# Optimization experiments

Hardware: AMD Instinct MI355X
Metric: run time of the kernel (lower is better)

## Reference

```python
import jax, jax.numpy as jnp
import numpy as np

EMB = 1024
HEADS = 16
HEAD_DIM = EMB // HEADS
FF = 4 * EMB
B, S = 4, 2048


def gelu_tanh(x):
    c = jnp.sqrt(jnp.asarray(2.0 / jnp.pi, x.dtype))
    return 0.5 * x * (1.0 + jnp.tanh(c * (x + 0.044715 * x ** 3)))


def layernorm(x, g, b, eps=1e-5):
    mu = jnp.mean(x, axis=-1, keepdims=True)
    var = jnp.var(x, axis=-1, keepdims=True)
    return (x - mu) * jax.lax.rsqrt(var + eps) * g + b


def setup_inputs() -> dict:
    key = jax.random.key(0)
    ks = jax.random.split(key, 12)
    s = 0.02
    return {
        "x": jax.random.normal(ks[0], (B, S, EMB), jnp.float32),
        "Wq": jax.random.normal(ks[1], (EMB, EMB), jnp.float32) * s,
        "bq": jnp.zeros((EMB,), jnp.float32),
        "Wk": jax.random.normal(ks[2], (EMB, EMB), jnp.float32) * s,
        "bk": jnp.zeros((EMB,), jnp.float32),
        "Wv": jax.random.normal(ks[3], (EMB, EMB), jnp.float32) * s,
        "bv": jnp.zeros((EMB,), jnp.float32),
        "Wo": jax.random.normal(ks[4], (EMB, EMB), jnp.float32) * s,
        "bo": jnp.zeros((EMB,), jnp.float32),
        "W1": jax.random.normal(ks[5], (EMB, FF), jnp.float32) * s,
        "b1": jnp.zeros((FF,), jnp.float32),
        "W2": jax.random.normal(ks[6], (FF, EMB), jnp.float32) * s,
        "b2": jnp.zeros((EMB,), jnp.float32),
        "g1": jnp.ones((EMB,), jnp.float32),
        "be1": jnp.zeros((EMB,), jnp.float32),
        "g2": jnp.ones((EMB,), jnp.float32),
        "be2": jnp.zeros((EMB,), jnp.float32),
    }


def reference(x, Wq, bq, Wk, bk, Wv, bv, Wo, bo, W1, b1, W2, b2, g1, be1, g2, be2):
    b, s, _ = x.shape
    shortcut = x
    h = layernorm(x, g1, be1)
    # QKV projections -> [b, heads, s, head_dim]
    def proj(W, bias):
        return (h @ W + bias).reshape(b, s, HEADS, HEAD_DIM).transpose(0, 2, 1, 3)
    q, k, v = proj(Wq, bq), proj(Wk, bk), proj(Wv, bv)
    scores = jnp.einsum('bhqd,bhkd->bhqk', q, k) / jnp.sqrt(jnp.asarray(HEAD_DIM, x.dtype))
    causal = jnp.triu(jnp.ones((s, s), bool), k=1)  # True above diagonal -> masked
    scores = jnp.where(causal, -jnp.inf, scores)
    probs = jax.nn.softmax(scores, axis=-1)  # dropout p=0 -> identity
    ctx = jnp.einsum('bhqk,bhkd->bhqd', probs, v).transpose(0, 2, 1, 3).reshape(b, s, EMB)
    attn_out = ctx @ Wo + bo
    x = attn_out + shortcut
    shortcut = x
    h = layernorm(x, g2, be2)
    ff = gelu_tanh(h @ W1 + b1) @ W2 + b2
    return ff + shortcut
```

## Files before the change

kernel.cpp:

```cpp
#include <hip/hip_runtime.h>
#include <hip/hip_bf16.h>

#define EMB 1024
#define HEADS 16
#define HDIM 64
#define FFDIM 4096
#define BSZ 4
#define SEQ 2048
#define MROWS (BSZ * SEQ)
#define QKVW 3072
#define VSTRIDE 2080

typedef __attribute__((ext_vector_type(8))) short bf16x8;
typedef __attribute__((ext_vector_type(4))) float f32x4;
typedef __attribute__((ext_vector_type(16))) float f32x16;
typedef __attribute__((ext_vector_type(4))) unsigned short u16x4;
typedef unsigned short u16;

__device__ __forceinline__ float bf2f(u16 u) {
  union { unsigned int i; float f; } c; c.i = ((unsigned int)u) << 16; return c.f;
}
__device__ __forceinline__ u16 f2bf(float f) {
  union { float f; unsigned int i; } c; c.f = f;
  unsigned int i = c.i + 0x7fff + ((c.i >> 16) & 1);
  return (u16)(i >> 16);
}
__device__ __forceinline__ unsigned fbits(float f) {
  union { float f; unsigned u; } c; c.f = f; return c.u;
}
__device__ __forceinline__ unsigned pk2(float e0, float e1) {
  return (fbits(e0) >> 16) | (fbits(e1) & 0xffff0000u);
}
__device__ __forceinline__ f32x16 zero16() {
  f32x16 z;
#pragma unroll
  for (int i = 0; i < 16; ++i) z[i] = 0.f;
  return z;
}
__device__ __forceinline__ void gload16(const u16* g, void* lds) {
  __builtin_amdgcn_global_load_lds(
      (const __attribute__((address_space(1))) void*)g,
      (__attribute__((address_space(3))) void*)lds, 16, 0, 0);
}

__global__ __launch_bounds__(256) void ln_kernel(
    const float* __restrict__ x, const float* __restrict__ g,
    const float* __restrict__ be, u16* __restrict__ out) {
  int w = threadIdx.x >> 6, l = threadIdx.x & 63;
  size_t row = (size_t)blockIdx.x * 4 + w;
  const float* xr = x + row * EMB;
  float f[4][4];
  float s = 0.f, s2 = 0.f;
#pragma unroll
  for (int c = 0; c < 4; ++c) {
    f32x4 v = *(const f32x4*)(xr + c * 256 + l * 4);
#pragma unroll
    for (int j = 0; j < 4; ++j) {
      f[c][j] = v[j];
      s += v[j];
      s2 += v[j] * v[j];
    }
  }
#pragma unroll
  for (int m = 1; m < 64; m <<= 1) {
    s  += __shfl_xor(s, m);
    s2 += __shfl_xor(s2, m);
  }
  float mu = s * (1.f / EMB);
  float var = s2 * (1.f / EMB) - mu * mu;
  float rs = rsqrtf(var + 1e-5f);
#pragma unroll
  for (int c = 0; c < 4; ++c) {
    u16x4 o;
#pragma unroll
    for (int j = 0; j < 4; ++j) {
      int col = c * 256 + l * 4 + j;
      o[j] = f2bf((f[c][j] - mu) * rs * g[col] + be[col]);
    }
    *(u16x4*)(out + row * EMB + c * 256 + l * 4) = o;
  }
}

__global__ __launch_bounds__(256) void transpose_cvt(
    const float* __restrict__ in, u16* __restrict__ out, int R, int C) {
  __shared__ u16 tile[32][33];
  int c0 = blockIdx.x * 32, r0 = blockIdx.y * 32;
  int tx = threadIdx.x, ty = threadIdx.y;
#pragma unroll
  for (int i = ty; i < 32; i += 8)
    tile[i][tx] = f2bf(in[(size_t)(r0 + i) * C + c0 + tx]);
  __syncthreads();
#pragma unroll
  for (int i = ty; i < 32; i += 8)
    out[(size_t)(c0 + i) * R + r0 + tx] = tile[tx][i];
}

__global__ __launch_bounds__(256) void concat_bias(
    const float* __restrict__ a, const float* __restrict__ b,
    const float* __restrict__ c, float* __restrict__ o) {
  int i = blockIdx.x * 256 + threadIdx.x;
  o[i] = i < 1024 ? a[i] : (i < 2048 ? b[i - 1024] : c[i - 2048]);
}

__global__ __launch_bounds__(256) void transpose_v(
    const u16* __restrict__ QKV, u16* __restrict__ Vt) {
  __shared__ u16 tile[32][33];
  int s0 = blockIdx.x * 32, d0 = blockIdx.y * 32, bh = blockIdx.z;
  int h = bh % HEADS, b = bh / HEADS;
  int tx = threadIdx.x, ty = threadIdx.y;
  const u16* src = QKV + (size_t)b * SEQ * QKVW + 2048 + h * HDIM;
  u16* dst = Vt + (size_t)bh * HDIM * VSTRIDE;
#pragma unroll
  for (int i = ty; i < 32; i += 8)
    tile[i][tx] = src[(size_t)(s0 + i) * QKVW + d0 + tx];
  __syncthreads();
#pragma unroll
  for (int i = ty; i < 32; i += 8)
    dst[(size_t)(d0 + i) * VSTRIDE + s0 + tx] = tile[tx][i];
}

__device__ __forceinline__ float gelu_f(float v) {
  float inner = 0.7978845608028654f * (v + 0.044715f * v * v * v);
  return 0.5f * v * (1.f + tanhf(inner));
}

template <int EPI, typename OT>
__global__ __launch_bounds__(512, 1) void gemm8(
    const u16* __restrict__ A, const u16* __restrict__ Bt,
    const float* __restrict__ bias, const float* __restrict__ res,
    OT* __restrict__ C, int N, int K) {
  __shared__ u16 lds[3 * 24576];
  int nbn = N >> 7;
  int cpx = gridDim.x >> 3;
  int bid = blockIdx.x;
  int logical = (bid & 7) * cpx + (bid >> 3);
  int mb = logical / nbn, nb = logical % nbn;
  int m0 = mb << 8, n0 = nb << 7;
  int t = threadIdx.x, w = t >> 6, l = t & 63;
  int lg = l >> 4, lc = l & 15;
  int wr = w >> 2, wc = w & 3;
  int NT = K >> 6;
  int rsub = (w << 3) + (l >> 3);
  int slot_st = (l & 7) ^ (l >> 3);

  f32x4 acc[8][2] = {};

#pragma unroll
  for (int tt = 0; tt < 2; ++tt) {
    u16* dst = lds + tt * 24576 + (w << 9);
#pragma unroll
    for (int s = 0; s < 6; ++s) {
      int row = (s << 6) + rsub;
      const u16* g = (s < 4)
          ? A + (size_t)(m0 + row) * K + (tt << 6) + (slot_st << 3)
          : Bt + (size_t)(n0 + row - 256) * K + (tt << 6) + (slot_st << 3);
      gload16(g, dst + (s << 12));
    }
  }
  asm volatile("s_waitcnt vmcnt(6)" ::: "memory");
  __builtin_amdgcn_s_barrier();

  for (int kt = 0; kt < NT; ++kt) {
    const u16* lb = lds + (kt % 3) * 24576;
    bool dost = (kt + 2) < NT;
    u16* sb = lds + ((kt + 2) % 3) * 24576 + (w << 9);
    int k2 = (kt + 2) << 6;

    if (dost) {
#pragma unroll
      for (int s = 0; s < 3; ++s) {
        int row = (s << 6) + rsub;
        gload16(A + (size_t)(m0 + row) * K + k2 + (slot_st << 3), sb + (s << 12));
      }
    }
    bf16x8 bfr[2][2];
#pragma unroll
    for (int j = 0; j < 2; ++j)
#pragma unroll
      for (int kk = 0; kk < 2; ++kk) {
        int row = 256 + (wc << 5) + (j << 4) + lc;
        int slot = ((kk << 2) + lg) ^ (lc & 7);
        bfr[j][kk] = *(const bf16x8*)(lb + row * 64 + (slot << 3));
      }
    bf16x8 afr[4][2];
#pragma unroll
    for (int i = 0; i < 4; ++i)
#pragma unroll
      for (int kk = 0; kk < 2; ++kk) {
        int row = (wr << 7) + (i << 4) + lc;
        int slot = ((kk << 2) + lg) ^ (lc & 7);
        afr[i][kk] = *(const bf16x8*)(lb + row * 64 + (slot << 3));
      }
    __builtin_amdgcn_s_barrier();
    __builtin_amdgcn_s_setprio(1);
#pragma unroll
    for (int i = 0; i < 4; ++i)
#pragma unroll
      for (int j = 0; j < 2; ++j)
#pragma unroll
        for (int kk = 0; kk < 2; ++kk)
          acc[i][j] = __builtin_amdgcn_mfma_f32_16x16x32_bf16(
              afr[i][kk], bfr[j][kk], acc[i][j], 0, 0, 0);
    __builtin_amdgcn_s_setprio(0);
    __builtin_amdgcn_s_barrier();

    if (dost) {
#pragma unroll
      for (int s = 3; s < 6; ++s) {
        int row = (s << 6) + rsub;
        const u16* g = (s < 4)
            ? A + (size_t)(m0 + row) * K + k2 + (slot_st << 3)
            : Bt + (size_t)(n0 + row - 256) * K + k2 + (slot_st << 3);
        gload16(g, sb + (s << 12));
      }
    }
    bf16x8 afr2[4][2];
#pragma unroll
    for (int i = 0; i < 4; ++i)
#pragma unroll
      for (int kk = 0; kk < 2; ++kk) {
        int row = (wr << 7) + ((i + 4) << 4) + lc;
        int slot = ((kk << 2) + lg) ^ (lc & 7);
        afr2[i][kk] = *(const bf16x8*)(lb + row * 64 + (slot << 3));
      }
    __builtin_amdgcn_s_barrier();
    __builtin_amdgcn_s_setprio(1);
#pragma unroll
    for (int i = 0; i < 4; ++i)
#pragma unroll
      for (int j = 0; j < 2; ++j)
#pragma unroll
        for (int kk = 0; kk < 2; ++kk)
          acc[i + 4][j] = __builtin_amdgcn_mfma_f32_16x16x32_bf16(
              afr2[i][kk], bfr[j][kk], acc[i + 4][j], 0, 0, 0);
    __builtin_amdgcn_s_setprio(0);
    if (dost)
      asm volatile("s_waitcnt vmcnt(6)" ::: "memory");
    else
      asm volatile("s_waitcnt vmcnt(0)" ::: "memory");
    __builtin_amdgcn_s_barrier();
  }

#pragma unroll
  for (int i = 0; i < 8; ++i)
#pragma unroll
    for (int j = 0; j < 2; ++j) {
      int col = n0 + (wc << 5) + (j << 4) + lc;
      float bcol = bias[col];
#pragma unroll
      for (int r = 0; r < 4; ++r) {
        int row = m0 + (wr << 7) + (i << 4) + (lg << 2) + r;
        float v = acc[i][j][r] + bcol;
        if (EPI & 2) v = gelu_f(v);
        if (EPI & 1) v += res[(size_t)row * N + col];
        if (sizeof(OT) == 2)
          C[(size_t)row * N + col] = (OT)f2bf(v);
        else
          C[(size_t)row * N + col] = (OT)v;
      }
    }
}

#define QKT32(ACCS, QF)                                                     \
  do {                                                                      \
    ACCS = zero16();                                                        \
    _Pragma("unroll") for (int s_ = 0; s_ < 4; ++s_)                        \
        ACCS = __builtin_amdgcn_mfma_f32_32x32x16_bf16(kf[s_], QF[s_],      \
                                                       ACCS, 0, 0, 0);      \
  } while (0)

#define ATTN_STEP(ACCS, M, L, O0, O1, DIAG)                                 \
  do {                                                                      \
    float e_[16];                                                           \
    float tm = -1e30f;                                                      \
    _Pragma("unroll") for (int i = 0; i < 16; ++i) {                        \
      float sv = ACCS[i];                                                   \
      if (DIAG) {                                                           \
        int kvl = (i & 3) + 8 * (i >> 2) + 4 * g;                           \
        if (kvl > lq) sv = -1e30f;                                          \
      }                                                                     \
      e_[i] = sv;                                                           \
      tm = fmaxf(tm, sv);                                                   \
    }                                                                       \
    tm = fmaxf(tm, __shfl_xor(tm, 32));                                     \
    float nm = fmaxf(M, tm);                                                \
    if (!__all(tm <= M)) {                                                  \
      float scl = __expf(M - nm);                                           \
      L *= scl;                                                             \
      _Pragma("unroll") for (int i = 0; i < 16; ++i) {                      \
        O0[i] *= scl;                                                       \
        O1[i] *= scl;                                                       \
      }                                                                     \
    }                                                                       \
    M = nm;                                                                 \
    float ts = 0.f;                                                         \
    _Pragma("unroll") for (int i = 0; i < 16; ++i) {                        \
      e_[i] = __expf(e_[i] - nm);                                           \
      ts += e_[i];                                                          \
    }                                                                       \
    ts += __shfl_xor(ts, 32);                                               \
    L += ts;                                                                \
    _Pragma("unroll") for (int s_ = 0; s_ < 2; ++s_) {                      \
      unsigned plo0 = pk2(e_[8 * s_ + 0], e_[8 * s_ + 1]);                  \
      unsigned plo1 = pk2(e_[8 * s_ + 2], e_[8 * s_ + 3]);                  \
      unsigned phi0 = pk2(e_[8 * s_ + 4], e_[8 * s_ + 5]);                  \
      unsigned phi1 = pk2(e_[8 * s_ + 6], e_[8 * s_ + 7]);                  \
      unsigned recv0 = __shfl_xor(g ? plo0 : phi0, 32);                     \
      unsigned recv1 = __shfl_xor(g ? plo1 : phi1, 32);                     \
      union { unsigned u[4]; bf16x8 v; } pf_;                               \
      pf_.u[0] = g ? recv0 : plo0;                                          \
      pf_.u[1] = g ? recv1 : plo1;                                          \
      pf_.u[2] = g ? phi0 : recv0;                                          \
      pf_.u[3] = g ? phi1 : recv1;                                          \
      O0 = __builtin_amdgcn_mfma_f32_32x32x16_bf16(vf[0][s_], pf_.v, O0,    \
                                                   0, 0, 0);                \
      O1 = __builtin_amdgcn_mfma_f32_32x32x16_bf16(vf[1][s_], pf_.v, O1,    \
                                                   0, 0, 0);                \
    }                                                                       \
  } while (0)

#define LOAD_KV(KV0)                                                        \
  do {                                                                      \
    _Pragma("unroll") for (int s_ = 0; s_ < 4; ++s_)                        \
        kf[s_] = *(const bf16x8*)(Kp + (size_t)((KV0) + lq) * QKVW +        \
                                  s_ * 16 + g * 8);                         \
    _Pragma("unroll") for (int d_ = 0; d_ < 2; ++d_)                        \
        _Pragma("unroll") for (int s_ = 0; s_ < 2; ++s_)                    \
            vf[d_][s_] = *(const bf16x8*)(Vt +                              \
                (size_t)(d_ * 32 + lq) * VSTRIDE + (KV0) + s_ * 16 + g * 8);\
  } while (0)

#define WRITE_OUT(O0, O1, L, WQ0)                                           \
  do {                                                                      \
    float inv = 1.f / L;                                                    \
    u16* orow = Op + (size_t)((WQ0) + lq) * EMB;                            \
    _Pragma("unroll") for (int dblk = 0; dblk < 2; ++dblk) {                \
      _Pragma("unroll") for (int p = 0; p < 8; ++p) {                       \
        int i0 = 2 * p;                                                     \
        int d = dblk * 32 + 2 * (p & 1) + 8 * (p >> 1) + 4 * g;             \
        float v0 = (dblk ? O1[i0] : O0[i0]) * inv;                          \
        float v1 = (dblk ? O1[i0 + 1] : O0[i0 + 1]) * inv;                  \
        unsigned wd = (unsigned)f2bf(v0) | ((unsigned)f2bf(v1) << 16);      \
        *(unsigned*)(orow + d) = wd;                                        \
      }                                                                     \
    }                                                                       \
  } while (0)

__global__ __launch_bounds__(256, 2) void attn_kernel(
    const u16* __restrict__ QKV, const u16* __restrict__ VtG,
    u16* __restrict__ O) {
  int t = threadIdx.x, w = t >> 6, l = t & 63;
  int lq = l & 31, g = l >> 5;
  int wid = blockIdx.x * 4 + w;
  int qi = wid & 31, bh = wid >> 5;
  int h = bh & (HEADS - 1), b = bh >> 4;
  int wq0a = qi * 32, wq0b = (63 - qi) * 32;
  int ntA = qi + 1, ntB = 64 - qi;
  const u16* Qp = QKV + (size_t)b * SEQ * QKVW + h * HDIM;
  const u16* Kp = QKV + (size_t)b * SEQ * QKVW + 1024 + h * HDIM;
  const u16* Vt = VtG + (size_t)bh * HDIM * VSTRIDE;
  u16* Op = O + (size_t)b * SEQ * EMB + h * HDIM;

  bf16x8 qfA[4], qfB[4];
#pragma unroll
  for (int s = 0; s < 4; ++s) {
    bf16x8 ra = *(const bf16x8*)(Qp + (size_t)(wq0a + lq) * QKVW + s * 16 + g * 8);
    bf16x8 rb = *(const bf16x8*)(Qp + (size_t)(wq0b + lq) * QKVW + s * 16 + g * 8);
#pragma unroll
    for (int j = 0; j < 8; ++j) {
      qfA[s][j] = (short)f2bf(bf2f((u16)ra[j]) * 0.125f);
      qfB[s][j] = (short)f2bf(bf2f((u16)rb[j]) * 0.125f);
    }
  }

  f32x16 oA0 = zero16(), oA1 = zero16(), oB0 = zero16(), oB1 = zero16();
  f32x16 sA, sB;
  float mA = -1e30f, lA = 0.f, mB = -1e30f, lB = 0.f;
  bf16x8 kf[4], vf[2][2];

  for (int ti = 0; ti < ntA; ++ti) {
    int kv0 = ti * 32;
    LOAD_KV(kv0);
    QKT32(sA, qfA);
    QKT32(sB, qfB);
    bool diagA = (ti == ntA - 1);
    ATTN_STEP(sA, mA, lA, oA0, oA1, diagA);
    ATTN_STEP(sB, mB, lB, oB0, oB1, false);
  }
  WRITE_OUT(oA0, oA1, lA, wq0a);
  for (int ti = ntA; ti < ntB; ++ti) {
    int kv0 = ti * 32;
    LOAD_KV(kv0);
    QKT32(sB, qfB);
    bool diagB = (ti == ntB - 1);
    ATTN_STEP(sB, mB, lB, oB0, oB1, diagB);
  }
  WRITE_OUT(oB0, oB1, lB, wq0b);
}

extern "C" void kernel_launch(void* const* d_in, const int* in_sizes, int n_in,
                              void* d_out, int out_size, void* d_ws, size_t ws_size,
                              hipStream_t stream) {
  (void)in_sizes; (void)n_in; (void)out_size; (void)ws_size;
  const float* x   = (const float*)d_in[0];
  const float* Wq  = (const float*)d_in[1];
  const float* bq  = (const float*)d_in[2];
  const float* Wk  = (const float*)d_in[3];
  const float* bk  = (const float*)d_in[4];
  const float* Wv  = (const float*)d_in[5];
  const float* bv  = (const float*)d_in[6];
  const float* Wo  = (const float*)d_in[7];
  const float* bo  = (const float*)d_in[8];
  const float* W1  = (const float*)d_in[9];
  const float* b1  = (const float*)d_in[10];
  const float* W2  = (const float*)d_in[11];
  const float* b2  = (const float*)d_in[12];
  const float* g1  = (const float*)d_in[13];
  const float* be1 = (const float*)d_in[14];
  const float* g2  = (const float*)d_in[15];
  const float* be2 = (const float*)d_in[16];

  char* ws = (char*)d_ws;
  const size_t MB = 1ull << 20;
  u16*   WqkvT = (u16*)(ws + 0 * MB);
  u16*   WoT   = (u16*)(ws + 6 * MB);
  u16*   W1T   = (u16*)(ws + 8 * MB);
  u16*   W2T   = (u16*)(ws + 16 * MB);
  float* bqkv  = (float*)(ws + 24 * MB);
  u16*   hbuf  = (u16*)(ws + 25 * MB);
  float* x1f   = (float*)(ws + 41 * MB);
  u16*   qkv   = (u16*)(ws + 73 * MB);
  u16*   VtG   = (u16*)(ws + 121 * MB);
  u16*   gbuf  = (u16*)(ws + 73 * MB);

  dim3 tb(32, 8);
  transpose_cvt<<<dim3(EMB / 32, EMB / 32), tb, 0, stream>>>(Wq, WqkvT, EMB, EMB);
  transpose_cvt<<<dim3(EMB / 32, EMB / 32), tb, 0, stream>>>(Wk, WqkvT + 1024 * 1024, EMB, EMB);
  transpose_cvt<<<dim3(EMB / 32, EMB / 32), tb, 0, stream>>>(Wv, WqkvT + 2 * 1024 * 1024, EMB, EMB);
  transpose_cvt<<<dim3(EMB / 32, EMB / 32), tb, 0, stream>>>(Wo, WoT, EMB, EMB);
  transpose_cvt<<<dim3(FFDIM / 32, EMB / 32), tb, 0, stream>>>(W1, W1T, EMB, FFDIM);
  transpose_cvt<<<dim3(EMB / 32, FFDIM / 32), tb, 0, stream>>>(W2, W2T, FFDIM, EMB);
  concat_bias<<<12, 256, 0, stream>>>(bq, bk, bv, bqkv);

  ln_kernel<<<MROWS / 4, 256, 0, stream>>>(x, g1, be1, hbuf);

  gemm8<0, u16><<<(MROWS / 256) * (QKVW / 128), 512, 0, stream>>>(
      hbuf, WqkvT, bqkv, nullptr, qkv, QKVW, EMB);

  transpose_v<<<dim3(SEQ / 32, HDIM / 32, BSZ * HEADS), tb, 0, stream>>>(qkv, VtG);

  attn_kernel<<<BSZ * HEADS * (SEQ / 64) / 4, 256, 0, stream>>>(qkv, VtG, hbuf);

  gemm8<1, float><<<(MROWS / 256) * (EMB / 128), 512, 0, stream>>>(
      hbuf, WoT, bo, x, x1f, EMB, EMB);

  ln_kernel<<<MROWS / 4, 256, 0, stream>>>(x1f, g2, be2, hbuf);

  gemm8<2, u16><<<(MROWS / 256) * (FFDIM / 128), 512, 0, stream>>>(
      hbuf, W1T, b1, nullptr, gbuf, FFDIM, EMB);
  gemm8<1, float><<<(MROWS / 256) * (EMB / 128), 512, 0, stream>>>(
      gbuf, W2T, b2, x1f, (float*)d_out, EMB, FFDIM);
}
```

Before: 448.0 us.

## Rewrite GEMM as 4-stage half-K pipeline with wider N tiles and templated M

Replaces the 3-buffer 64-wide-K GEMM with a 4-deep ring of 32-wide-K half stages. Each stage has one barrier per step, and the next loads are issued right after the barrier. The tile changes from 256x128 to (MFR*32)x256. The Wo and W2 GEMMs use 128-row tiles so there are enough blocks to fill the chip. The aim is to hide more global-load latency and raise MFMA reuse per LDS fragment, at the cost of more accumulator registers and a new swizzle and waitcnt accounting that must be exactly right.

Result: slower. 474.2 us (+5.9%).

```diff
diff --git a/kernel.cpp b/kernel.cpp
--- a/kernel.cpp
+++ b/kernel.cpp
@@ -124,133 +124,101 @@
   return 0.5f * v * (1.f + tanhf(inner));
 }
 
-template <int EPI, typename OT>
-__global__ __launch_bounds__(512, 1) void gemm8(
+template <int MFR, int EPI, typename OT>
+__global__ __launch_bounds__(512, 1) void gemm_p(
     const u16* __restrict__ A, const u16* __restrict__ Bt,
     const float* __restrict__ bias, const float* __restrict__ res,
     OT* __restrict__ C, int N, int K) {
-  __shared__ u16 lds[3 * 24576];
-  int nbn = N >> 7;
+  constexpr int BM = MFR * 32;
+  constexpr int HHALF = (BM + 256) * 32;
+  constexpr int NA = MFR / 2;
+  constexpr int LPH = NA + 2;
+  __shared__ u16 lds[4 * HHALF];
+  int nbn = N >> 8;
   int cpx = gridDim.x >> 3;
   int bid = blockIdx.x;
   int logical = (bid & 7) * cpx + (bid >> 3);
   int mb = logical / nbn, nb = logical % nbn;
-  int m0 = mb << 8, n0 = nb << 7;
+  int m0 = mb * BM, n0 = nb << 8;
   int t = threadIdx.x, w = t >> 6, l = t & 63;
   int lg = l >> 4, lc = l & 15;
   int wr = w >> 2, wc = w & 3;
-  int NT = K >> 6;
-  int rsub = (w << 3) + (l >> 3);
-  int slot_st = (l & 7) ^ (l >> 3);
-
-  f32x4 acc[8][2] = {};
-
-#pragma unroll
-  for (int tt = 0; tt < 2; ++tt) {
-    u16* dst = lds + tt * 24576 + (w << 9);
-#pragma unroll
-    for (int s = 0; s < 6; ++s) {
-      int row = (s << 6) + rsub;
-      const u16* g = (s < 4)
-          ? A + (size_t)(m0 + row) * K + (tt << 6) + (slot_st << 3)
-          : Bt + (size_t)(n0 + row - 256) * K + (tt << 6) + (slot_st << 3);
-      gload16(g, dst + (s << 12));
-    }
-  }
-  asm volatile("s_waitcnt vmcnt(6)" ::: "memory");
+  int NT = K >> 6, NH = NT * 2;
+  f32x4 acc[MFR][4] = {};
+
+  auto stage = [&](int H) {
+    int kb = (H >> 1) * 64 + (H & 1) * 32;
+    char* hb = (char*)lds + (H & 3) * (HHALF * 2);
+#pragma unroll
+    for (int i = 0; i < NA; ++i) {
+      int q = i * 512 + t;
+      int r = q >> 2, p = q & 3;
+      int kc = kb + ((p ^ ((r >> 1) & 3)) << 3);
+      gload16(A + (size_t)(m0 + r) * K + kc, hb + i * 8192 + w * 1024);
+    }
+#pragma unroll
+    for (int i = 0; i < 2; ++i) {
+      int q = i * 512 + t;
+      int r = q >> 2, p = q & 3;
+      int kc = kb + ((p ^ ((r >> 1) & 3)) << 3);
+      gload16(Bt + (size_t)(n0 + r) * K + kc, hb + BM * 64 + i * 8192 + w * 1024);
+    }
+  };
+
+  stage(0); stage(1); stage(2); stage(3);
+  if constexpr (LPH == 4) asm volatile("s_waitcnt vmcnt(8)" ::: "memory");
+  else                    asm volatile("s_waitcnt vmcnt(6)" ::: "memory");
   __builtin_amdgcn_s_barrier();
-
-  for (int kt = 0; kt < NT; ++kt) {
-    const u16* lb = lds + (kt % 3) * 24576;
-    bool dost = (kt + 2) < NT;
-    u16* sb = lds + ((kt + 2) % 3) * 24576 + (w << 9);
-    int k2 = (kt + 2) << 6;
-
-    if (dost) {
-#pragma unroll
-      for (int s = 0; s < 3; ++s) {
-        int row = (s << 6) + rsub;
-        gload16(A + (size_t)(m0 + row) * K + k2 + (slot_st << 3), sb + (s << 12));
+  __builtin_amdgcn_sched_barrier(0);
+
+  for (int h = 0; h < NH; ++h) {
+    const u16* lb = lds + (h & 3) * HHALF;
+    bf16x8 bfr[4], afr[MFR];
+#pragma unroll
+    for (int n = 0; n < 4; ++n) {
+      int rb = (wc << 6) + (n << 4) + lc;
+      bfr[n] = *(const bf16x8*)(lb + BM * 32 + rb * 32 + ((lg ^ ((rb >> 1) & 3)) << 3));
+    }
+#pragma unroll
+    for (int m = 0; m < MFR; ++m) {
+      int ra = wr * (MFR * 16) + (m << 4) + lc;
+      afr[m] = *(const bf16x8*)(lb + ra * 32 + ((lg ^ ((ra >> 1) & 3)) << 3));
+    }
+    __builtin_amdgcn_s_setprio(1);
+#pragma unroll
+    for (int m = 0; m < MFR; ++m)
+#pragma unroll
+      for (int n = 0; n < 4; ++n)
+        acc[m][n] = __builtin_amdgcn_mfma_f32_16x16x32_bf16(
+            afr[m], bfr[n], acc[m][n], 0, 0, 0);
+    __builtin_amdgcn_s_setprio(0);
+    if (h < NH - 1) {
+      int rem = NH - 2 - h;
+      if (rem >= 2) {
+        if constexpr (LPH == 4) asm volatile("s_waitcnt vmcnt(8)" ::: "memory");
+        else                    asm volatile("s_waitcnt vmcnt(6)" ::: "memory");
+      } else if (rem == 1) {
+        if constexpr (LPH == 4) asm volatile("s_waitcnt vmcnt(4)" ::: "memory");
+        else                    asm volatile("s_waitcnt vmcnt(3)" ::: "memory");
+      } else {
+        asm volatile("s_waitcnt vmcnt(0)" ::: "memory");
       }
-    }
-    bf16x8 bfr[2][2];
-#pragma unroll
-    for (int j = 0; j < 2; ++j)
-#pragma unroll
-      for (int kk = 0; kk < 2; ++kk) {
-        int row = 256 + (wc << 5) + (j << 4) + lc;
-        int slot = ((kk << 2) + lg) ^ (lc & 7);
-        bfr[j][kk] = *(const bf16x8*)(lb + row * 64 + (slot << 3));
-      }
-    bf16x8 afr[4][2];
-#pragma unroll
-    for (int i = 0; i < 4; ++i)
-#pragma unroll
-      for (int kk = 0; kk < 2; ++kk) {
-        int row = (wr << 7) + (i << 4) + lc;
-        int slot = ((kk << 2) + lg) ^ (lc & 7);
-        afr[i][kk] = *(const bf16x8*)(lb + row * 64 + (slot << 3));
-      }
-    __builtin_amdgcn_s_barrier();
-    __builtin_amdgcn_s_setprio(1);
-#pragma unroll
-    for (int i = 0; i < 4; ++i)
-#pragma unroll
-      for (int j = 0; j < 2; ++j)
-#pragma unroll
-        for (int kk = 0; kk < 2; ++kk)
-          acc[i][j] = __builtin_amdgcn_mfma_f32_16x16x32_bf16(
-              afr[i][kk], bfr[j][kk], acc[i][j], 0, 0, 0);
-    __builtin_amdgcn_s_setprio(0);
-    __builtin_amdgcn_s_barrier();
-
-    if (dost) {
-#pragma unroll
-      for (int s = 3; s < 6; ++s) {
-        int row = (s << 6) + rsub;
-        const u16* g = (s < 4)
-            ? A + (size_t)(m0 + row) * K + k2 + (slot_st << 3)
-            : Bt + (size_t)(n0 + row - 256) * K + k2 + (slot_st << 3);
-        gload16(g, sb + (s << 12));
-      }
-    }
-    bf16x8 afr2[4][2];
-#pragma unroll
-    for (int i = 0; i < 4; ++i)
-#pragma unroll
-      for (int kk = 0; kk < 2; ++kk) {
-        int row = (wr << 7) + ((i + 4) << 4) + lc;
-        int slot = ((kk << 2) + lg) ^ (lc & 7);
-        afr2[i][kk] = *(const bf16x8*)(lb + row * 64 + (slot << 3));
-      }
-    __builtin_amdgcn_s_barrier();
-    __builtin_amdgcn_s_setprio(1);
-#pragma unroll
-    for (int i = 0; i < 4; ++i)
-#pragma unroll
-      for (int j = 0; j < 2; ++j)
-#pragma unroll
-        for (int kk = 0; kk < 2; ++kk)
-          acc[i + 4][j] = __builtin_amdgcn_mfma_f32_16x16x32_bf16(
-              afr2[i][kk], bfr[j][kk], acc[i + 4][j], 0, 0, 0);
-    __builtin_amdgcn_s_setprio(0);
-    if (dost)
-      asm volatile("s_waitcnt vmcnt(6)" ::: "memory");
-    else
-      asm volatile("s_waitcnt vmcnt(0)" ::: "memory");
-    __builtin_amdgcn_s_barrier();
-  }
-
-#pragma unroll
-  for (int i = 0; i < 8; ++i)
-#pragma unroll
-    for (int j = 0; j < 2; ++j) {
-      int col = n0 + (wc << 5) + (j << 4) + lc;
+      __builtin_amdgcn_s_barrier();
+      __builtin_amdgcn_sched_barrier(0);
+      if (h + 4 < NH) stage(h + 4);
+    }
+  }
+
+#pragma unroll
+  for (int m = 0; m < MFR; ++m)
+#pragma unroll
+    for (int n = 0; n < 4; ++n) {
+      int col = n0 + (wc << 6) + (n << 4) + lc;
       float bcol = bias[col];
 #pragma unroll
       for (int r = 0; r < 4; ++r) {
-        int row = m0 + (wr << 7) + (i << 4) + (lg << 2) + r;
-        float v = acc[i][j][r] + bcol;
+        int row = m0 + wr * (MFR * 16) + (m << 4) + (lg << 2) + r;
+        float v = acc[m][n][r] + bcol;
         if (EPI & 2) v = gelu_f(v);
         if (EPI & 1) v += res[(size_t)row * N + col];
         if (sizeof(OT) == 2)
@@ -444,20 +412,20 @@
 
   ln_kernel<<<MROWS / 4, 256, 0, stream>>>(x, g1, be1, hbuf);
 
-  gemm8<0, u16><<<(MROWS / 256) * (QKVW / 128), 512, 0, stream>>>(
+  gemm_p<8, 0, u16><<<(MROWS / 256) * (QKVW / 256), 512, 0, stream>>>(
       hbuf, WqkvT, bqkv, nullptr, qkv, QKVW, EMB);
 
   transpose_v<<<dim3(SEQ / 32, HDIM / 32, BSZ * HEADS), tb, 0, stream>>>(qkv, VtG);
 
   attn_kernel<<<BSZ * HEADS * (SEQ / 64) / 4, 256, 0, stream>>>(qkv, VtG, hbuf);
 
-  gemm8<1, float><<<(MROWS / 256) * (EMB / 128), 512, 0, stream>>>(
+  gemm_p<4, 1, float><<<(MROWS / 128) * (EMB / 256), 512, 0, stream>>>(
       hbuf, WoT, bo, x, x1f, EMB, EMB);
 
   ln_kernel<<<MROWS / 4, 256, 0, stream>>>(x1f, g2, be2, hbuf);
 
-  gemm8<2, u16><<<(MROWS / 256) * (FFDIM / 128), 512, 0, stream>>>(
+  gemm_p<8, 2, u16><<<(MROWS / 256) * (FFDIM / 256), 512, 0, stream>>>(
       hbuf, W1T, b1, nullptr, gbuf, FFDIM, EMB);
-  gemm8<1, float><<<(MROWS / 256) * (EMB / 128), 512, 0, stream>>>(
+  gemm_p<4, 1, float><<<(MROWS / 128) * (EMB / 256), 512, 0, stream>>>(
       gbuf, W2T, b2, x1f, (float*)d_out, EMB, FFDIM);
 }
```
